# Kernel tuning notes

Measured on AMD Instinct MI355X. Metric: run time of the kernel, lower is better.

## Reference

```python
import jax, jax.numpy as jnp
import numpy as np

B, S, DM = 2, 2048, 1024
H, HD = 16, 64  # heads, head_dims = dims // heads
SCALE = HD ** -0.5


def softmax_one(x):
    # softmax with +1 in the denominator: exp(x_i) / (1 + sum_j exp(x_j))
    # stable form: shift by m = max(max(x), 0)
    m = jnp.maximum(jnp.max(x, axis=-1, keepdims=True), 0.0)
    e = jnp.exp(x - m)
    return e / (jnp.exp(-m) + jnp.sum(e, axis=-1, keepdims=True))


def setup_inputs() -> dict:
    key = jax.random.key(0)
    ks = jax.random.split(key, 11)
    init = lambda k, shape, fan_in: jax.random.uniform(k, shape, jnp.float32, -1.0, 1.0) * (fan_in ** -0.5)
    return {
        "query": jax.random.normal(ks[0], (B, S, DM), jnp.float32),
        "key": jax.random.normal(ks[1], (B, S, DM), jnp.float32),
        "value": jax.random.normal(ks[2], (B, S, DM), jnp.float32),
        "Wq": init(ks[3], (H * HD, DM), DM), "bq": init(ks[4], (H * HD,), DM),
        "Wk": init(ks[5], (H * HD, DM), DM), "bk": init(ks[6], (H * HD,), DM),
        "Wv": init(ks[7], (H * HD, DM), DM), "bv": init(ks[8], (H * HD,), DM),
        "Wo": init(ks[9], (DM, H * HD), H * HD), "bo": init(ks[10], (DM,), H * HD),
    }


def _proj(x, W, b):
    # [B,S,DM] -> [B,H,S,HD]
    y = x @ W.T + b
    return y.reshape(B, S, H, HD).transpose(0, 2, 1, 3)


def reference(query, key, value, Wq, bq, Wk, bk, Wv, bv, Wo, bo):
    Q = _proj(query, Wq, bq)
    K = _proj(key, Wk, bk)
    V = _proj(value, Wv, bv)
    scores = jnp.einsum("bhqd,bhkd->bhqk", Q, K) * SCALE  # [B,H,S,S]
    attn = softmax_one(scores)
    out = jnp.einsum("bhqk,bhkd->bhqd", attn, V)  # [B,H,S,HD]
    out = out.transpose(0, 2, 1, 3).reshape(B, S, H * HD)
    return out @ Wo.T + bo
```

## Files before the change

kernel.cpp:

```cpp
#include <hip/hip_runtime.h>

#define B_ 2
#define S_ 2048
#define DM_ 1024
#define H_ 16
#define HD_ 64
#define QSCALE_ 0.18033688011112042f

typedef __bf16 bf16;
typedef __attribute__((ext_vector_type(4))) __bf16 bf16x4;
typedef __attribute__((ext_vector_type(8))) __bf16 bf16x8;
typedef __attribute__((ext_vector_type(4))) float f32x4;

#define MFMA16(a, b, c) __builtin_amdgcn_mfma_f32_16x16x32_bf16((a), (b), (c), 0, 0, 0)
#define EXP2(x) __builtin_amdgcn_exp2f(x)

__device__ __forceinline__ void async16(const bf16* g, bf16* l) {
  __builtin_amdgcn_global_load_lds(
      (const __attribute__((address_space(1))) void*)g,
      (__attribute__((address_space(3))) void*)l, 16, 0, 0);
}

__global__ __launch_bounds__(256) void convert_kernel(
    const float* __restrict__ q, const float* __restrict__ k,
    const float* __restrict__ v, const float* __restrict__ wq,
    const float* __restrict__ wk, const float* __restrict__ wv,
    const float* __restrict__ wo, bf16* __restrict__ dst) {
  size_t idx = ((size_t)blockIdx.x * 256 + threadIdx.x) * 8;
  const float* src;
  size_t off;
  if (idx < 4194304) { src = q; off = idx; }
  else if (idx < 8388608) { src = k; off = idx - 4194304; }
  else if (idx < 12582912) { src = v; off = idx - 8388608; }
  else if (idx < 13631488) { src = wq; off = idx - 12582912; }
  else if (idx < 14680064) { src = wk; off = idx - 13631488; }
  else if (idx < 15728640) { src = wv; off = idx - 14680064; }
  else { src = wo; off = idx - 15728640; }
  float4 a = *(const float4*)(src + off);
  float4 b = *(const float4*)(src + off + 4);
  bf16x8 o;
  o[0] = (bf16)a.x; o[1] = (bf16)a.y; o[2] = (bf16)a.z; o[3] = (bf16)a.w;
  o[4] = (bf16)b.x; o[5] = (bf16)b.y; o[6] = (bf16)b.z; o[7] = (bf16)b.w;
  *(bf16x8*)(dst + idx) = o;
}

template <int MODE>
__device__ __forceinline__ void gemm_body(bf16* smem, const bf16* A,
                                          const bf16* W, const float* bias,
                                          bf16* C, float scale, int m0,
                                          int n0) {
  constexpr int K = 1024;
  bf16* As = smem;
  bf16* Bs = smem + 128 * 64;
  const int t = threadIdx.x;
  const int lane = t & 63, wave = t >> 6;
  const int quad = lane >> 4, l16 = lane & 15;
  const int wm = (wave >> 1) * 64, wn = (wave & 1) * 64;

  const f32x4 zero = {0.f, 0.f, 0.f, 0.f};
  f32x4 acc[4][4];
  for (int i = 0; i < 4; i++)
    for (int j = 0; j < 4; j++) acc[i][j] = zero;

  for (int k0 = 0; k0 < K; k0 += 64) {
    for (int i = 0; i < 4; ++i) {
      int c = i * 256 + t;
      int row = c >> 3, g = c & 7;
      int off = k0 + ((g ^ (row & 7)) * 8);
      async16(A + (size_t)(m0 + row) * K + off, As + c * 8);
      async16(W + (size_t)(n0 + row) * K + off, Bs + c * 8);
    }
    __syncthreads();

    for (int ks = 0; ks < 2; ks++) {
      bf16x8 af[4], bfr[4];
      for (int mb = 0; mb < 4; mb++) {
        int ra = wm + mb * 16 + l16;
        af[mb] = *(const bf16x8*)(As + ra * 64 + ((ks * 4 + quad) ^ (ra & 7)) * 8);
        int rb = wn + mb * 16 + l16;
        bfr[mb] = *(const bf16x8*)(Bs + rb * 64 + ((ks * 4 + quad) ^ (rb & 7)) * 8);
      }
      for (int mb = 0; mb < 4; mb++)
        for (int nb = 0; nb < 4; nb++)
          acc[mb][nb] = MFMA16(af[mb], bfr[nb], acc[mb][nb]);
    }
    __syncthreads();
  }

  if constexpr (MODE == 2) {
    bf16* Ct = smem;
    for (int nb = 0; nb < 4; nb++) {
      int cl = wn + nb * 16 + l16;
      float bv = bias[n0 + cl] * scale;
      for (int mb = 0; mb < 4; mb++) {
        int rowb = wm + mb * 16 + quad * 4;
        bf16x4 v;
        for (int r = 0; r < 4; r++)
          v[r] = (bf16)(acc[mb][nb][r] * scale + bv);
        *(bf16x4*)(Ct + cl * 136 + rowb) = v;
      }
    }
    __syncthreads();
    int c = t >> 1, half = t & 1;
    int colg = n0 + c;
    int hh = colg >> 6, dd = colg & 63;
    int bb = m0 >> 11, s0 = m0 & (S_ - 1);
    bf16* dst = C + (((size_t)(bb * H_ + hh)) * HD_ + dd) * S_ + s0 + half * 64;
    const bf16* srcr = Ct + c * 136 + half * 64;
    for (int j = 0; j < 8; ++j)
      *(bf16x8*)(dst + j * 8) = *(const bf16x8*)(srcr + j * 8);
  } else {
    for (int nb = 0; nb < 4; nb++) {
      int col = n0 + wn + nb * 16 + l16;
      float bv = bias[col] * scale;
      for (int mb = 0; mb < 4; mb++) {
        int rowb = m0 + wm + mb * 16 + quad * 4;
        for (int r = 0; r < 4; r++) {
          int row = rowb + r;
          float o = acc[mb][nb][r] * scale + bv;
          int bb = row >> 11, s = row & (S_ - 1);
          int h = col >> 6, d = col & 63;
          C[(((size_t)(bb * H_ + h)) * S_ + s) * HD_ + d] = (bf16)o;
        }
      }
    }
  }
}

__global__ __launch_bounds__(256, 4) void qkv_proj_kernel(
    const bf16* Xc, const float* bq, const float* bk, const float* bv,
    bf16* Qo, bf16* Ko, bf16* Vo) {
  __shared__ __align__(16) bf16 smem[128 * 136];
  int bid = blockIdx.x;
  int z = bid >> 8;
  int r = bid & 255;
  int c = r & 7;
  int j = r >> 3;
  int m0 = (c * 4 + (j & 3)) * 128;
  int n0 = (j >> 2) * 128;
  const bf16* A = Xc + (size_t)z * 4194304;
  const bf16* W = Xc + 12582912 + (size_t)z * 1048576;
  if (z == 0)
    gemm_body<1>(smem, A, W, bq, Qo, QSCALE_, m0, n0);
  else if (z == 1)
    gemm_body<1>(smem, A, W, bk, Ko, 1.0f, m0, n0);
  else
    gemm_body<2>(smem, A, W, bv, Vo, 1.0f, m0, n0);
}

__global__ __launch_bounds__(256, 4) void out_proj_kernel(const bf16* A,
                                                          const bf16* W,
                                                          const float* bias,
                                                          float* C) {
  constexpr int K = 1024, N = 1024;
  __shared__ __align__(16) bf16 As[128 * 64];
  __shared__ __align__(16) bf16 Bs[64 * 64];
  const int t = threadIdx.x;
  const int lane = t & 63, wave = t >> 6;
  const int quad = lane >> 4, l16 = lane & 15;
  int bid = blockIdx.x;
  int c = bid & 7;
  int j = bid >> 3;
  const int m0 = (c * 4 + (j & 3)) * 128;
  const int n0 = (j >> 2) * 64;
  const int wm = wave * 32;

  const f32x4 zero = {0.f, 0.f, 0.f, 0.f};
  f32x4 acc[2][4];
  for (int i = 0; i < 2; i++)
    for (int jn = 0; jn < 4; jn++) acc[i][jn] = zero;

  for (int k0 = 0; k0 < K; k0 += 64) {
    for (int i = 0; i < 4; ++i) {
      int cc = i * 256 + t;
      int row = cc >> 3, g = cc & 7;
      int off = k0 + ((g ^ (row & 7)) * 8);
      async16(A + (size_t)(m0 + row) * K + off, As + cc * 8);
    }
    for (int i = 0; i < 2; ++i) {
      int cc = i * 256 + t;
      int row = cc >> 3, g = cc & 7;
      int off = k0 + ((g ^ (row & 7)) * 8);
      async16(W + (size_t)(n0 + row) * K + off, Bs + cc * 8);
    }
    __syncthreads();

    for (int ks = 0; ks < 2; ks++) {
      bf16x8 af[2], bfr[4];
      for (int mb = 0; mb < 2; mb++) {
        int ra = wm + mb * 16 + l16;
        af[mb] = *(const bf16x8*)(As + ra * 64 + ((ks * 4 + quad) ^ (ra & 7)) * 8);
      }
      for (int nb = 0; nb < 4; nb++) {
        int rb = nb * 16 + l16;
        bfr[nb] =
            *(const bf16x8*)(Bs + rb * 64 + ((ks * 4 + quad) ^ (rb & 7)) * 8);
      }
      for (int mb = 0; mb < 2; mb++)
        for (int nb = 0; nb < 4; nb++)
          acc[mb][nb] = MFMA16(af[mb], bfr[nb], acc[mb][nb]);
    }
    __syncthreads();
  }

  for (int nb = 0; nb < 4; nb++) {
    int col = n0 + nb * 16 + l16;
    float bv = bias[col];
    for (int mb = 0; mb < 2; mb++) {
      int rowb = m0 + wm + mb * 16 + quad * 4;
      for (int r = 0; r < 4; r++)
        C[(size_t)(rowb + r) * N + col] = acc[mb][nb][r] + bv;
    }
  }
}

__global__ __launch_bounds__(256, 2) void attn_kernel(
    const bf16* __restrict__ Q, const bf16* __restrict__ Kg,
    const bf16* __restrict__ VTg, bf16* __restrict__ O) {
  __shared__ __align__(16) bf16 Ks[128 * 64];
  __shared__ __align__(16) bf16 Vt[64 * 128];
  __shared__ __align__(16) bf16 Ps[4 * 64 * 72];
  __shared__ float rsL[2][64];
  const int t = threadIdx.x;
  const int lane = t & 63, wave = t >> 6;
  const int quad = lane >> 4, l16 = lane & 15;
  const int id = blockIdx.x;
  const int bh = id & 31;
  const int qt = id >> 5;
  const int q0 = qt * 128;
  const int b = bh >> 4, h = bh & 15;
  const int qhalf = wave >> 1, khalf = wave & 1;
  const size_t base = ((size_t)(b * H_ + h)) * S_ * HD_;
  const bf16* Qp = Q + base;
  const bf16* Kp = Kg + base;
  const bf16* Vp = VTg + base;

  bf16x8 aq[4][2];
  for (int s = 0; s < 4; s++) {
    const bf16* qr = Qp + (size_t)(q0 + qhalf * 64 + s * 16 + l16) * HD_;
    aq[s][0] = *(const bf16x8*)(qr + quad * 8);
    aq[s][1] = *(const bf16x8*)(qr + 32 + quad * 8);
  }

  const f32x4 zero = {0.f, 0.f, 0.f, 0.f};
  f32x4 oc[4][4];
  for (int s = 0; s < 4; s++)
    for (int d = 0; d < 4; d++) oc[s][d] = zero;
  float rs[4] = {0.f, 0.f, 0.f, 0.f};

  bf16* Pw = Ps + wave * (64 * 72);

  for (int kv0 = 0; kv0 < S_; kv0 += 128) {
    for (int i = 0; i < 4; ++i) {
      int c = i * 256 + t;
      int row = c >> 3, g = c & 7;
      async16(Kp + (size_t)(kv0 + row) * HD_ + (g ^ (row & 7)) * 8, Ks + c * 8);
    }
    for (int i = 0; i < 4; ++i) {
      int c = i * 256 + t;
      int d = c >> 4, g = c & 15;
      async16(Vp + (size_t)d * S_ + kv0 + (g ^ (d & 15)) * 8, Vt + c * 8);
    }
    __syncthreads();

    f32x4 sc[4][4];
    for (int s = 0; s < 4; s++)
      for (int nb = 0; nb < 4; nb++) sc[s][nb] = zero;
    for (int ks = 0; ks < 2; ks++) {
      for (int nb = 0; nb < 4; nb++) {
        int row = khalf * 64 + nb * 16 + l16;
        int slot = (ks * 4 + quad) ^ (row & 7);
        bf16x8 kf = *(const bf16x8*)(Ks + row * 64 + slot * 8);
        __builtin_amdgcn_s_setprio(1);
        for (int s = 0; s < 4; s++)
          sc[s][nb] = MFMA16(kf, aq[s][ks], sc[s][nb]);
        __builtin_amdgcn_s_setprio(0);
      }
    }

    for (int s = 0; s < 4; s++) {
      bf16* prow = Pw + (s * 16 + l16) * 72 + quad * 4;
      for (int nb = 0; nb < 4; nb++) {
        float p0 = EXP2(sc[s][nb][0]);
        float p1 = EXP2(sc[s][nb][1]);
        float p2 = EXP2(sc[s][nb][2]);
        float p3 = EXP2(sc[s][nb][3]);
        rs[s] += (p0 + p1) + (p2 + p3);
        bf16x4 pv = {(bf16)p0, (bf16)p1, (bf16)p2, (bf16)p3};
        *(bf16x4*)(prow + nb * 16) = pv;
      }
    }

    for (int ks2 = 0; ks2 < 2; ks2++) {
      bf16x8 vf[4];
      for (int db = 0; db < 4; db++) {
        int row = db * 16 + l16;
        int g = khalf * 8 + ks2 * 4 + quad;
        vf[db] = *(const bf16x8*)(Vt + row * 128 + (g ^ (row & 15)) * 8);
      }
      for (int s = 0; s < 4; s++) {
        bf16x8 ap =
            *(const bf16x8*)(Pw + (s * 16 + l16) * 72 + ks2 * 32 + quad * 8);
        __builtin_amdgcn_s_setprio(1);
        for (int db = 0; db < 4; db++)
          oc[s][db] = MFMA16(ap, vf[db], oc[s][db]);
        __builtin_amdgcn_s_setprio(0);
      }
    }

    __syncthreads();
  }

  float* Ld = (float*)Ps;
  if (khalf) {
    for (int s = 0; s < 4; s++) {
      float rtot = rs[s];
      rtot += __shfl_xor(rtot, 16);
      rtot += __shfl_xor(rtot, 32);
      if (quad == 0) rsL[qhalf][s * 16 + l16] = rtot;
      for (int db = 0; db < 4; db++)
        for (int r = 0; r < 4; r++)
          Ld[(size_t)qhalf * (64 * 68) + (s * 16 + quad * 4 + r) * 68 +
             db * 16 + l16] = oc[s][db][r];
    }
  }
  __syncthreads();
  if (!khalf) {
    for (int s = 0; s < 4; s++) {
      float rtot = rs[s];
      rtot += __shfl_xor(rtot, 16);
      rtot += __shfl_xor(rtot, 32);
      float l_all = 1.f + rtot + rsL[qhalf][s * 16 + l16];
      for (int r = 0; r < 4; r++) {
        float inv = 1.f / __shfl(l_all, quad * 4 + r);
        int qrow = q0 + qhalf * 64 + s * 16 + quad * 4 + r;
        size_t orow = ((size_t)(b * S_ + qrow) * H_ + h) * HD_;
        for (int db = 0; db < 4; db++) {
          float val = oc[s][db][r] +
                      Ld[(size_t)qhalf * (64 * 68) +
                         (s * 16 + quad * 4 + r) * 68 + db * 16 + l16];
          O[orow + db * 16 + l16] = (bf16)(val * inv);
        }
      }
    }
  }
}

extern "C" void kernel_launch(void* const* d_in, const int* in_sizes, int n_in,
                              void* d_out, int out_size, void* d_ws,
                              size_t ws_size, hipStream_t stream) {
  const float* query = (const float*)d_in[0];
  const float* key = (const float*)d_in[1];
  const float* value = (const float*)d_in[2];
  const float* bq = (const float*)d_in[4];
  const float* bk = (const float*)d_in[6];
  const float* bv = (const float*)d_in[8];
  const float* bo = (const float*)d_in[10];
  float* out = (float*)d_out;

  bf16* Xc = (bf16*)d_ws;
  bf16* Qw = Xc + 16777216;
  const size_t SZ = (size_t)B_ * H_ * S_ * HD_;
  bf16* Kw = Qw + SZ;
  bf16* Vw = Kw + SZ;
  bf16* Ow = Vw + SZ;

  convert_kernel<<<8192, 256, 0, stream>>>(query, key, value,
                                           (const float*)d_in[3],
                                           (const float*)d_in[5],
                                           (const float*)d_in[7],
                                           (const float*)d_in[9], Xc);
  qkv_proj_kernel<<<768, 256, 0, stream>>>(Xc, bq, bk, bv, Qw, Kw, Vw);
  attn_kernel<<<512, 256, 0, stream>>>(Qw, Kw, Vw, Ow);
  out_proj_kernel<<<512, 256, 0, stream>>>(Ow, Xc + 15728640, bo, out);
}
```

Baseline: 205.8 us.

## Keep softmax probabilities in registers by permuting the PV reduction order

The exponentiated scores now stay in registers: the QK^T output fragments are packed straight into bf16x8 A-operands for the PV MFMA, instead of going through a per-wave LDS buffer. To make this legal, the kv reduction index is permuted, and V fragments are gathered with two bf16x4 LDS reads each to match. This removes the P store/load round-trip through LDS and shrinks shared memory to one buffer reused for the final cross-wave reduction. The cost is twice as many, narrower V reads from LDS.

```diff
diff --git a/kernel.cpp b/kernel.cpp
--- a/kernel.cpp
+++ b/kernel.cpp
@@ -217,10 +217,9 @@
 __global__ __launch_bounds__(256, 2) void attn_kernel(
     const bf16* __restrict__ Q, const bf16* __restrict__ Kg,
     const bf16* __restrict__ VTg, bf16* __restrict__ O) {
-  __shared__ __align__(16) bf16 Ks[128 * 64];
-  __shared__ __align__(16) bf16 Vt[64 * 128];
-  __shared__ __align__(16) bf16 Ps[4 * 64 * 72];
-  __shared__ float rsL[2][64];
+  __shared__ __align__(16) bf16 smem[17152];
+  bf16* Ks = smem;
+  bf16* Vt = smem + 8192;
   const int t = threadIdx.x;
   const int lane = t & 63, wave = t >> 6;
   const int quad = lane >> 4, l16 = lane & 15;
@@ -248,8 +247,6 @@
     for (int d = 0; d < 4; d++) oc[s][d] = zero;
   float rs[4] = {0.f, 0.f, 0.f, 0.f};
 
-  bf16* Pw = Ps + wave * (64 * 72);
-
   for (int kv0 = 0; kv0 < S_; kv0 += 128) {
     for (int i = 0; i < 4; ++i) {
       int c = i * 256 + t;
@@ -278,32 +275,42 @@
       }
     }
 
+    bf16x8 pa8[4][2];
     for (int s = 0; s < 4; s++) {
-      bf16* prow = Pw + (s * 16 + l16) * 72 + quad * 4;
-      for (int nb = 0; nb < 4; nb++) {
-        float p0 = EXP2(sc[s][nb][0]);
-        float p1 = EXP2(sc[s][nb][1]);
-        float p2 = EXP2(sc[s][nb][2]);
-        float p3 = EXP2(sc[s][nb][3]);
-        rs[s] += (p0 + p1) + (p2 + p3);
-        bf16x4 pv = {(bf16)p0, (bf16)p1, (bf16)p2, (bf16)p3};
-        *(bf16x4*)(prow + nb * 16) = pv;
-      }
-    }
-
-    for (int ks2 = 0; ks2 < 2; ks2++) {
-      bf16x8 vf[4];
+      for (int p = 0; p < 2; p++) {
+        bf16x8 v8;
+        for (int hh = 0; hh < 2; hh++) {
+          int nb = p * 2 + hh;
+          float p0 = EXP2(sc[s][nb][0]);
+          float p1 = EXP2(sc[s][nb][1]);
+          float p2 = EXP2(sc[s][nb][2]);
+          float p3 = EXP2(sc[s][nb][3]);
+          rs[s] += (p0 + p1) + (p2 + p3);
+          v8[hh * 4 + 0] = (bf16)p0;
+          v8[hh * 4 + 1] = (bf16)p1;
+          v8[hh * 4 + 2] = (bf16)p2;
+          v8[hh * 4 + 3] = (bf16)p3;
+        }
+        pa8[s][p] = v8;
+      }
+    }
+
+    for (int p = 0; p < 2; p++) {
+      bf16x8 vf8[4];
       for (int db = 0; db < 4; db++) {
         int row = db * 16 + l16;
-        int g = khalf * 8 + ks2 * 4 + quad;
-        vf[db] = *(const bf16x8*)(Vt + row * 128 + (g ^ (row & 15)) * 8);
+        int glo = khalf * 8 + 4 * p + (quad >> 1);
+        int sub = (quad & 1) * 4;
+        bf16x4 lo =
+            *(const bf16x4*)(Vt + row * 128 + ((glo ^ (row & 15)) * 8) + sub);
+        bf16x4 hi = *(const bf16x4*)(Vt + row * 128 +
+                                     (((glo + 2) ^ (row & 15)) * 8) + sub);
+        vf8[db] = __builtin_shufflevector(lo, hi, 0, 1, 2, 3, 4, 5, 6, 7);
       }
       for (int s = 0; s < 4; s++) {
-        bf16x8 ap =
-            *(const bf16x8*)(Pw + (s * 16 + l16) * 72 + ks2 * 32 + quad * 8);
         __builtin_amdgcn_s_setprio(1);
         for (int db = 0; db < 4; db++)
-          oc[s][db] = MFMA16(ap, vf[db], oc[s][db]);
+          oc[s][db] = MFMA16(pa8[s][p], vf8[db], oc[s][db]);
         __builtin_amdgcn_s_setprio(0);
       }
     }
@@ -311,34 +318,37 @@
     __syncthreads();
   }
 
-  float* Ld = (float*)Ps;
+  float rtot[4];
+  for (int s = 0; s < 4; s++) {
+    float v = rs[s];
+    v += __shfl_xor(v, 16);
+    v += __shfl_xor(v, 32);
+    rtot[s] = v;
+  }
+
+  float* Ld = (float*)smem;
+  float* rsL = (float*)smem + 2 * 64 * 66;
   if (khalf) {
     for (int s = 0; s < 4; s++) {
-      float rtot = rs[s];
-      rtot += __shfl_xor(rtot, 16);
-      rtot += __shfl_xor(rtot, 32);
-      if (quad == 0) rsL[qhalf][s * 16 + l16] = rtot;
+      if (quad == 0) rsL[qhalf * 64 + s * 16 + l16] = rtot[s];
       for (int db = 0; db < 4; db++)
         for (int r = 0; r < 4; r++)
-          Ld[(size_t)qhalf * (64 * 68) + (s * 16 + quad * 4 + r) * 68 +
+          Ld[(size_t)qhalf * (64 * 66) + (s * 16 + quad * 4 + r) * 66 +
              db * 16 + l16] = oc[s][db][r];
     }
   }
   __syncthreads();
   if (!khalf) {
     for (int s = 0; s < 4; s++) {
-      float rtot = rs[s];
-      rtot += __shfl_xor(rtot, 16);
-      rtot += __shfl_xor(rtot, 32);
-      float l_all = 1.f + rtot + rsL[qhalf][s * 16 + l16];
+      float l_all = 1.f + rtot[s] + rsL[qhalf * 64 + s * 16 + l16];
       for (int r = 0; r < 4; r++) {
         float inv = 1.f / __shfl(l_all, quad * 4 + r);
         int qrow = q0 + qhalf * 64 + s * 16 + quad * 4 + r;
         size_t orow = ((size_t)(b * S_ + qrow) * H_ + h) * HD_;
         for (int db = 0; db < 4; db++) {
           float val = oc[s][db][r] +
-                      Ld[(size_t)qhalf * (64 * 68) +
-                         (s * 16 + quad * 4 + r) * 68 + db * 16 + l16];
+                      Ld[(size_t)qhalf * (64 * 66) +
+                         (s * 16 + quad * 4 + r) * 66 + db * 16 + l16];
           O[orow + db * 16 + l16] = (bf16)(val * inv);
         }
       }
```

Result: faster. 199.5 us (-3.1%).
